# Kernel tuning notes

Hardware: AMD Instinct MI355X
Metric: run time of the kernel (lower is better)

Reference implementation:

```python
import jax, jax.numpy as jnp
import numpy as np

B, H, W, C = 16, 64, 64, 256
HEADS, WS, SHIFTS, QD = 8, 8, (0, 4), 512
N = WS * WS
HD = C // HEADS
MLP_H = 4 * C
DEPTH = 2
EPS = 1e-5


def _rel_pos_index():
    coords = np.stack(np.meshgrid(np.arange(WS), np.arange(WS), indexing='ij'))  # [2,ws,ws]
    flat = coords.reshape(2, -1)
    rel = (flat[:, :, None] - flat[:, None, :]).transpose(1, 2, 0)  # [N,N,2]
    rel[..., 0] += WS - 1
    rel[..., 1] += WS - 1
    rel[..., 0] *= 2 * WS - 1
    return jnp.asarray(rel.sum(-1))  # [N,N] int


def _shift_mask(shift):
    img = np.zeros((H, W))
    cnt = 0
    for hs in (slice(0, -WS), slice(-WS, -shift), slice(-shift, None)):
        for ws_ in (slice(0, -WS), slice(-WS, -shift), slice(-shift, None)):
            img[hs, ws_] = cnt
            cnt += 1
    mw = img.reshape(H // WS, WS, W // WS, WS).transpose(0, 2, 1, 3).reshape(-1, N)  # [nW,N]
    am = mw[:, None, :] - mw[:, :, None]
    return jnp.asarray(np.where(am != 0, -100.0, 0.0).astype(np.float32))  # [nW,N,N]


RPI = _rel_pos_index()


def layernorm(x, g, b):
    mu = x.mean(-1, keepdims=True)
    var = ((x - mu) ** 2).mean(-1, keepdims=True)
    return (x - mu) * jax.lax.rsqrt(var + EPS) * g + b


def window_partition(x):  # [B,H,W,C] -> [B*nW, N, C]
    x = x.reshape(B, H // WS, WS, W // WS, WS, C)
    return x.transpose(0, 1, 3, 2, 4, 5).reshape(-1, N, C)


def window_reverse(w):  # [B*nW, N, C] -> [B,H,W,C]
    x = w.reshape(B, H // WS, W // WS, WS, WS, C)
    return x.transpose(0, 1, 3, 2, 4, 5).reshape(B, H, W, C)


def swin_block(x, shift, n1g, n1b, qkvw, qkvb, rpb, pw, pb, n2g, n2b, f1w, f1b, f2w, f2b):
    shortcut = x
    y = layernorm(x, n1g, n1b).reshape(B, H, W, C)
    if shift > 0:
        y = jnp.roll(y, (-shift, -shift), axis=(1, 2))
    xw = window_partition(y)                                      # [B_, N, C]
    qkv = (xw @ qkvw + qkvb).reshape(-1, N, 3, HEADS, HD)
    q, k, v = (qkv[:, :, i].transpose(0, 2, 1, 3) for i in range(3))  # [B_,h,N,hd]
    scores = jnp.einsum('bhnd,bhmd->bhnm', q * (HD ** -0.5), k)
    bias = rpb[RPI].transpose(2, 0, 1)                            # [h,N,N]
    scores = scores + bias[None]
    if shift > 0:
        mask = _shift_mask(shift)                                 # [nW,N,N]
        nW = mask.shape[0]
        scores = scores.reshape(B, nW, HEADS, N, N) + mask[None, :, None]
        scores = scores.reshape(-1, HEADS, N, N)
    attn = jax.nn.softmax(scores, axis=-1)
    out = jnp.einsum('bhnm,bhmd->bhnd', attn, v).transpose(0, 2, 1, 3).reshape(-1, N, C)
    out = out @ pw + pb
    y = window_reverse(out)
    if shift > 0:
        y = jnp.roll(y, (shift, shift), axis=(1, 2))
    x = shortcut + y.reshape(B, H * W, C)
    h = layernorm(x, n2g, n2b)
    h = jax.nn.gelu(h @ f1w + f1b, approximate=False) @ f2w + f2b
    return x + h


def cross_attn(x, cond, cng, cnb, inw, inb, outw, outb):
    xn = layernorm(x, cng, cnb)
    q = xn @ inw[:C].T + inb[:C]
    k = cond @ inw[C:2 * C].T + inb[C:2 * C]
    v = cond @ inw[2 * C:].T + inb[2 * C:]
    Tq, Tk = q.shape[1], k.shape[1]
    q = q.reshape(B, Tq, HEADS, HD).transpose(0, 2, 1, 3) * (HD ** -0.5)
    k = k.reshape(B, Tk, HEADS, HD).transpose(0, 2, 1, 3)
    v = v.reshape(B, Tk, HEADS, HD).transpose(0, 2, 1, 3)
    a = jax.nn.softmax(jnp.einsum('bhqd,bhkd->bhqk', q, k), axis=-1)
    o = jnp.einsum('bhqk,bhkd->bhqd', a, v).transpose(0, 2, 1, 3).reshape(B, Tq, C)
    return x + o @ outw.T + outb


def setup_inputs() -> dict:
    key = jax.random.key(0)
    ks = iter(jax.random.split(key, 40))
    s = 0.02
    d = {
        'x': jax.random.normal(next(ks), (B, H * W, C), jnp.float32),
        'emb': jax.random.normal(next(ks), (B, 1, QD), jnp.float32),
        'qenc_w': jax.random.normal(next(ks), (QD, C)) * s,
        'qenc_b': jnp.zeros((C,)),
        'n1_g': jnp.ones((DEPTH, C)), 'n1_b': jnp.zeros((DEPTH, C)),
        'qkv_w': jax.random.normal(next(ks), (DEPTH, C, 3 * C)) * s,
        'qkv_b': jnp.zeros((DEPTH, 3 * C)),
        'rpb': jax.random.normal(next(ks), (DEPTH, (2 * WS - 1) ** 2, HEADS)) * s,
        'proj_w': jax.random.normal(next(ks), (DEPTH, C, C)) * s,
        'proj_b': jnp.zeros((DEPTH, C)),
        'n2_g': jnp.ones((DEPTH, C)), 'n2_b': jnp.zeros((DEPTH, C)),
        'fc1_w': jax.random.normal(next(ks), (DEPTH, C, MLP_H)) * s,
        'fc1_b': jnp.zeros((DEPTH, MLP_H)),
        'fc2_w': jax.random.normal(next(ks), (DEPTH, MLP_H, C)) * s,
        'fc2_b': jnp.zeros((DEPTH, C)),
        'cn_g': jnp.ones((DEPTH, C)), 'cn_b': jnp.zeros((DEPTH, C)),
        'ca_in_w': jax.random.normal(next(ks), (DEPTH, 3 * C, C)) * s,
        'ca_in_b': jnp.zeros((DEPTH, 3 * C)),
        'ca_out_w': jax.random.normal(next(ks), (DEPTH, C, C)) * s,
        'ca_out_b': jnp.zeros((DEPTH, C)),
    }
    return d


def reference(x, emb, qenc_w, qenc_b, n1_g, n1_b, qkv_w, qkv_b, rpb, proj_w, proj_b,
              n2_g, n2_b, fc1_w, fc1_b, fc2_w, fc2_b, cn_g, cn_b,
              ca_in_w, ca_in_b, ca_out_w, ca_out_b):
    for d in range(DEPTH):
        x = swin_block(x, SHIFTS[d], n1_g[d], n1_b[d], qkv_w[d], qkv_b[d], rpb[d],
                       proj_w[d], proj_b[d], n2_g[d], n2_b[d],
                       fc1_w[d], fc1_b[d], fc2_w[d], fc2_b[d])
        cond = emb @ qenc_w + qenc_b  # recomputed per block as in original
        x = cross_attn(x, cond, cn_g[d], cn_b[d], ca_in_w[d], ca_in_b[d],
                       ca_out_w[d], ca_out_b[d])
    return x
```

## Files before the change

kernel.cpp:

```cpp
#include <hip/hip_runtime.h>


typedef unsigned short bfraw;
typedef short s16x8 __attribute__((ext_vector_type(8)));
typedef short s16x4 __attribute__((ext_vector_type(4)));
typedef float f32x4 __attribute__((ext_vector_type(4)));

#define DEV static __device__ __forceinline__

DEV float b2f(int u){
  union { unsigned int i; float f; } x;
  x.i = ((unsigned int)u & 0xffffu) << 16;
  return x.f;
}
DEV unsigned short f2bbits(float f){
  union { float f; unsigned int i; } x; x.f = f;
  unsigned int i = x.i;
  unsigned int lsb = (i >> 16) & 1u;
  i += 0x7fffu + lsb;
  return (unsigned short)(i >> 16);
}
DEV float gelu_tanh(float x){
  float t2 = 1.5957691216057308f * fmaf(0.044715f * x * x, x, x);
  float e = __expf(-t2);
  return x * __builtin_amdgcn_rcpf(1.f + e);
}

#define GLOAD_LDS16(g, l) __builtin_amdgcn_global_load_lds(                      \
    (const __attribute__((address_space(1))) void*)(g),                          \
    (__attribute__((address_space(3))) void*)(l), 16, 0, 0)

__global__ void k_tr(const float* __restrict__ in, bfraw* __restrict__ out, int K, int N){
  int idx = blockIdx.x * 256 + threadIdx.x;
  if (idx >= K * N) return;
  int n = idx / K, k = idx - n * K;
  out[idx] = f2bbits(in[(size_t)k * N + n]);
}

__global__ __launch_bounds__(256) void k_ln(
    const float* __restrict__ x, const float* __restrict__ g,
    const float* __restrict__ b, bfraw* __restrict__ y)
{
  const int lane = threadIdx.x & 63, wv = threadIdx.x >> 6;
  const size_t row = (size_t)blockIdx.x * 4 + wv;
  const float4 v = *(const float4*)(x + row * 256 + lane * 4);
  float s  = v.x + v.y + v.z + v.w;
  float s2 = v.x*v.x + v.y*v.y + v.z*v.z + v.w*v.w;
#pragma unroll
  for (int off = 32; off; off >>= 1){
    s  += __shfl_xor(s,  off);
    s2 += __shfl_xor(s2, off);
  }
  float mu  = s * (1.f/256.f);
  float var = s2 * (1.f/256.f) - mu * mu;
  float rs  = rsqrtf(var + 1e-5f);
  const float4 gv = *(const float4*)(g + lane * 4);
  const float4 bv = *(const float4*)(b + lane * 4);
  s16x4 o;
  o[0] = (short)f2bbits((v.x - mu) * rs * gv.x + bv.x);
  o[1] = (short)f2bbits((v.y - mu) * rs * gv.y + bv.y);
  o[2] = (short)f2bbits((v.z - mu) * rs * gv.z + bv.z);
  o[3] = (short)f2bbits((v.w - mu) * rs * gv.w + bv.w);
  *(s16x4*)(y + row * 256 + lane * 4) = o;
}

template<int EPI>
__global__ __launch_bounds__(256, 2) void k_gemm(
    const bfraw* __restrict__ A, const bfraw* __restrict__ Bt,
    const float* __restrict__ bias,
    bfraw* __restrict__ Cout, int ldc,
    float* __restrict__ xfp, const float* __restrict__ xin,
    const float* __restrict__ addv,
    int M, int N, int K, int shift)
{
  constexpr int BK = 64;
  __shared__ __align__(16) bfraw sA[2][128 * BK];
  __shared__ __align__(16) bfraw sB[2][128 * BK];
  const int tid = threadIdx.x, lane = tid & 63, w = tid >> 6;
  const int lo16 = lane & 15, hg = lane >> 4;
  const int nbm = M >> 7, nbn = N >> 7;
  const int nwg = nbm * nbn;
  const int bid = blockIdx.x;
  const int wgid = (bid & 7) * (nwg >> 3) + (bid >> 3);
  const int tn = wgid % nbn, tm = wgid / nbn;
  const int m0 = tm << 7, n0 = tn << 7;
  const int wm = w & 1, wn = w >> 1;
  f32x4 acc[4][4] = {};

  const int srow = (w << 5) + (lane >> 3);
  const int scol = (((lane & 7) ^ (lane >> 3)) << 3);
  const int ksw  = (lane & 7) << 3;
  const bfraw* gA = A  + (size_t)(m0 + srow) * K + scol;
  const bfraw* gB = Bt + (size_t)(n0 + srow) * K + scol;

  const int cb = n0 + (wn << 6) + 4 * hg;

  f32x4 bv4[4];
#pragma unroll
  for (int ni = 0; ni < 4; ++ni) bv4[ni] = *(const f32x4*)(bias + cb + ni * 16);
  size_t rowoff_[4];
  f32x4 pre[16], pav[4];
  if constexpr (EPI == 2 || EPI == 3){
#pragma unroll
    for (int mi = 0; mi < 4; ++mi){
      const int r = m0 + (wm << 6) + (mi << 4) + lo16;
      if constexpr (EPI == 2){
        int b_ = r >> 12, rem = r & 4095;
        int wi = rem >> 6, n_ = rem & 63;
        int gi = ((wi >> 3) * 8 + (n_ >> 3) + shift) & 63;
        int gj = ((wi & 7) * 8 + (n_ & 7) + shift) & 63;
        rowoff_[mi] = ((size_t)b_ << 12) + gi * 64 + gj;
      } else {
        rowoff_[mi] = (size_t)r;
      }
      const float* src = (EPI == 2 ? xin : (const float*)xfp) + rowoff_[mi] * 256 + cb;
#pragma unroll
      for (int ni = 0; ni < 4; ++ni)
        pre[mi * 4 + ni] = *(const f32x4*)(src + ni * 16);
    }
    if constexpr (EPI == 3){
      const float* av = addv + (size_t)(m0 >> 12) * 256 + cb;
#pragma unroll
      for (int ni = 0; ni < 4; ++ni) pav[ni] = *(const f32x4*)(av + ni * 16);
    }
  }

  const int nt = K / BK;
#pragma unroll
  for (int i = 0; i < 4; ++i){
    GLOAD_LDS16(gA + (size_t)(i * 8) * K, &sA[0][(w * 4 + i) * 512]);
    GLOAD_LDS16(gB + (size_t)(i * 8) * K, &sB[0][(w * 4 + i) * 512]);
  }
  for (int t = 0; t < nt; ++t){
    __syncthreads();
    const int cur = t & 1;
    if (t + 1 < nt){
      const int nxt = cur ^ 1, kt = (t + 1) * BK;
#pragma unroll
      for (int i = 0; i < 4; ++i){
        GLOAD_LDS16(gA + (size_t)(i * 8) * K + kt, &sA[nxt][(w * 4 + i) * 512]);
        GLOAD_LDS16(gB + (size_t)(i * 8) * K + kt, &sB[nxt][(w * 4 + i) * 512]);
      }
    }
#pragma unroll
    for (int ks = 0; ks < 2; ++ks){
      const int ko = (ks * 32 + (hg << 3)) ^ ksw;
      s16x8 af[4], bfr[4];
#pragma unroll
      for (int i = 0; i < 4; ++i){
        af[i]  = *(const s16x8*)&sA[cur][((wm << 6) + (i << 4) + lo16) * BK + ko];
        bfr[i] = *(const s16x8*)&sB[cur][((wn << 6) + (i << 4) + lo16) * BK + ko];
      }
#pragma unroll
      for (int ni = 0; ni < 4; ++ni)
#pragma unroll
        for (int mi = 0; mi < 4; ++mi)
          acc[ni][mi] = __builtin_amdgcn_mfma_f32_16x16x32_bf16(
              bfr[ni], af[mi], acc[ni][mi], 0, 0, 0);
    }
  }

#pragma unroll
  for (int mi = 0; mi < 4; ++mi){
    if constexpr (EPI == 0 || EPI == 1){
      const int r = m0 + (wm << 6) + (mi << 4) + lo16;
      bfraw* crow = Cout + (size_t)r * ldc + cb;
#pragma unroll
      for (int ni = 0; ni < 4; ++ni){
        f32x4 v = acc[ni][mi] + bv4[ni];
        s16x4 o;
#pragma unroll
        for (int j = 0; j < 4; ++j){
          float val = v[j];
          if constexpr (EPI == 1) val = gelu_tanh(val);
          o[j] = (short)f2bbits(val);
        }
        *(s16x4*)(crow + ni * 16) = o;
      }
    } else if constexpr (EPI == 2){
      float* xo = xfp + rowoff_[mi] * 256 + cb;
#pragma unroll
      for (int ni = 0; ni < 4; ++ni)
        *(f32x4*)(xo + ni * 16) = acc[ni][mi] + bv4[ni] + pre[mi * 4 + ni];
    } else {
      float* xo = xfp + rowoff_[mi] * 256 + cb;
#pragma unroll
      for (int ni = 0; ni < 4; ++ni)
        *(f32x4*)(xo + ni * 16) = acc[ni][mi] + bv4[ni] + pre[mi * 4 + ni] + pav[ni];
    }
  }
}

__global__ __launch_bounds__(64) void k_bias(const float* __restrict__ rpb,
                                             float* __restrict__ biasPk)
{
  const int blk = blockIdx.x;
  const int d = blk >> 5, cls = (blk >> 3) & 3, h = blk & 7;
  const int l = threadIdx.x, lo16 = l & 15, hg = l >> 4;
  const float* rp = rpb + (size_t)d * 225 * 8;
  float* ob = biasPk + (((size_t)d * 4 + cls) * 8 + h) * 4096;
#pragma unroll
  for (int mi = 0; mi < 4; ++mi)
#pragma unroll
    for (int ni = 0; ni < 4; ++ni)
#pragma unroll
      for (int j = 0; j < 4; ++j){
        int k = 16 * mi + 4 * hg + j, q = 16 * ni + lo16;
        int qr = q >> 3, qc = q & 7, kr = k >> 3, kc = k & 7;
        float v = rp[((qr - kr + 7) * 15 + (qc - kc + 7)) * 8 + h];
        if (d == 1){
          int lq = ((cls >> 1) ? (qr < 4 ? 1 : 2) : 0) * 3 + ((cls & 1) ? (qc < 4 ? 1 : 2) : 0);
          int lk = ((cls >> 1) ? (kr < 4 ? 1 : 2) : 0) * 3 + ((cls & 1) ? (kc < 4 ? 1 : 2) : 0);
          if (lq != lk) v -= 100.f;
        }
        ob[(mi * 4 + ni) * 256 + l * 4 + j] = v;
      }
}

__global__ __launch_bounds__(64) void k_attn(
    const bfraw* __restrict__ qkv, const float* __restrict__ biasPk,
    bfraw* __restrict__ aout, int shift)
{
  __shared__ __align__(16) bfraw sV[64 * 32];
  __shared__ __align__(16) bfraw sP[64 * 64];
  const int win = blockIdx.x >> 3, h = blockIdx.x & 7;
  const int b = win >> 6, wr = (win >> 3) & 7, wc = win & 7;
  const int l = threadIdx.x, lo16 = l & 15, hg = l >> 4;

  auto grow_of = [&](int n) -> size_t {
    int gi = (wr * 8 + (n >> 3) + shift) & 63;
    int gj = (wc * 8 + (n & 7) + shift) & 63;
    return ((size_t)b << 12) + gi * 64 + gj;
  };

  s16x8 vreg[4];
#pragma unroll
  for (int i = 0; i < 4; ++i){
    int row = i * 16 + (l >> 2);
    vreg[i] = *(const s16x8*)(qkv + grow_of(row) * 768 + 512 + h * 32 + (l & 3) * 8);
  }
#pragma unroll
  for (int i = 0; i < 4; ++i)
    *(s16x8*)&sV[i * 512 + l * 8] = vreg[i];

  s16x8 aK[4], bQ[4];
#pragma unroll
  for (int t = 0; t < 4; ++t){
    const bfraw* base = qkv + grow_of(16 * t + lo16) * 768 + h * 32 + hg * 8;
    bQ[t] = *(const s16x8*)base;
    aK[t] = *(const s16x8*)(base + 256);
  }

  f32x4 acc[4][4] = {};
#pragma unroll
  for (int mi = 0; mi < 4; ++mi)
#pragma unroll
    for (int ni = 0; ni < 4; ++ni)
      acc[mi][ni] = __builtin_amdgcn_mfma_f32_16x16x32_bf16(aK[mi], bQ[ni], acc[mi][ni], 0, 0, 0);

  const int cls = ((wr == 7) ? 2 : 0) | ((wc == 7) ? 1 : 0);
  const float* bb = biasPk + ((size_t)(cls * 8 + h)) * 4096;
#pragma unroll
  for (int mi = 0; mi < 4; ++mi)
#pragma unroll
    for (int ni = 0; ni < 4; ++ni){
      f32x4 bv4 = *(const f32x4*)(bb + (mi * 4 + ni) * 256 + l * 4);
      acc[mi][ni] = acc[mi][ni] * 0.17677669529663689f + bv4;
    }

#pragma unroll
  for (int ni = 0; ni < 4; ++ni){
    float m = acc[0][ni][0];
#pragma unroll
    for (int mi = 0; mi < 4; ++mi)
#pragma unroll
      for (int j = 0; j < 4; ++j) m = fmaxf(m, acc[mi][ni][j]);
    m = fmaxf(m, __shfl_xor(m, 16));
    m = fmaxf(m, __shfl_xor(m, 32));
    float s = 0.f;
#pragma unroll
    for (int mi = 0; mi < 4; ++mi)
#pragma unroll
      for (int j = 0; j < 4; ++j){
        float e = __expf(acc[mi][ni][j] - m);
        acc[mi][ni][j] = e; s += e;
      }
    s += __shfl_xor(s, 16);
    s += __shfl_xor(s, 32);
    float inv = 1.f / s;
#pragma unroll
    for (int mi = 0; mi < 4; ++mi)
#pragma unroll
      for (int j = 0; j < 4; ++j) acc[mi][ni][j] *= inv;
  }

#pragma unroll
  for (int mi = 0; mi < 4; ++mi)
#pragma unroll
    for (int ni = 0; ni < 4; ++ni){
      unsigned int w0, w1;
      asm("v_cvt_pk_bf16_f32 %0, %1, %2" : "=v"(w0) : "v"(acc[mi][ni][0]), "v"(acc[mi][ni][1]));
      asm("v_cvt_pk_bf16_f32 %0, %1, %2" : "=v"(w1) : "v"(acc[mi][ni][2]), "v"(acc[mi][ni][3]));
      int q = 16 * ni + lo16;
      int ad = (q * 128 + (16 * mi + 4 * hg) * 2) ^ ((q & 7) << 4);
      *(uint2*)((char*)sP + ad) = make_uint2(w0, w1);
    }

  asm volatile("s_waitcnt lgkmcnt(0)" ::: "memory");
  __builtin_amdgcn_sched_barrier(0);

  f32x4 opv[4][2] = {};
#pragma unroll
  for (int kt = 0; kt < 2; ++kt){
    s16x8 ap[4];
#pragma unroll
    for (int qi = 0; qi < 4; ++qi){
      int q = 16 * qi + lo16;
      int ad = (q * 128 + (kt * 32 + hg * 8) * 2) ^ ((q & 7) << 4);
      ap[qi] = *(const s16x8*)((const char*)sP + ad);
    }
    s16x8 vb[2];
#pragma unroll
    for (int nt = 0; nt < 2; ++nt)
#pragma unroll
      for (int e = 0; e < 8; ++e)
        vb[nt][e] = (short)sV[(kt * 32 + hg * 8 + e) * 32 + nt * 16 + lo16];
#pragma unroll
    for (int qi = 0; qi < 4; ++qi)
#pragma unroll
      for (int nt = 0; nt < 2; ++nt)
        opv[qi][nt] = __builtin_amdgcn_mfma_f32_16x16x32_bf16(ap[qi], vb[nt], opv[qi][nt], 0, 0, 0);
  }

  bfraw* ob = aout + ((size_t)win * 64) * 256 + h * 32 + lo16;
#pragma unroll
  for (int qi = 0; qi < 4; ++qi)
#pragma unroll
    for (int nt = 0; nt < 2; ++nt)
#pragma unroll
      for (int j = 0; j < 4; ++j)
        ob[(size_t)(16 * qi + 4 * hg + j) * 256 + nt * 16] = f2bbits(opv[qi][nt][j]);
}

__global__ __launch_bounds__(256) void k_addvec(
    const float* __restrict__ emb, const float* __restrict__ qw, const float* __restrict__ qb,
    const float* __restrict__ inw, const float* __restrict__ inb,
    const float* __restrict__ outw, const float* __restrict__ outb,
    float* __restrict__ addv)
{
  const int d = blockIdx.x >> 4, b = blockIdx.x & 15;
  const int j = threadIdx.x;
  __shared__ float sc[256], sv[256];
  float a = qb[j];
  for (int k = 0; k < 512; ++k) a = fmaf(emb[b * 512 + k], qw[k * 256 + j], a);
  sc[j] = a; __syncthreads();
  float v = inb[d * 768 + 512 + j];
  const float* wrp = inw + (size_t)d * 768 * 256 + (size_t)(512 + j) * 256;
  for (int k = 0; k < 256; ++k) v = fmaf(sc[k], wrp[k], v);
  sv[j] = v; __syncthreads();
  float o = outb[d * 256 + j];
  const float* wop = outw + (size_t)d * 65536 + (size_t)j * 256;
  for (int k = 0; k < 256; ++k) o = fmaf(sv[k], wop[k], o);
  addv[(size_t)(d * 16 + b) * 256 + j] = o;
}

extern "C" void kernel_launch(void* const* d_in, const int* in_sizes, int n_in,
                              void* d_out, int out_size, void* d_ws, size_t ws_size,
                              hipStream_t stream)
{
  (void)in_sizes; (void)n_in; (void)out_size; (void)ws_size;
  const float* x_in     = (const float*)d_in[0];
  const float* emb      = (const float*)d_in[1];
  const float* qenc_w   = (const float*)d_in[2];
  const float* qenc_b   = (const float*)d_in[3];
  const float* n1_g     = (const float*)d_in[4];
  const float* n1_b     = (const float*)d_in[5];
  const float* qkv_w    = (const float*)d_in[6];
  const float* qkv_b    = (const float*)d_in[7];
  const float* rpb      = (const float*)d_in[8];
  const float* proj_w   = (const float*)d_in[9];
  const float* proj_b   = (const float*)d_in[10];
  const float* n2_g     = (const float*)d_in[11];
  const float* n2_b     = (const float*)d_in[12];
  const float* fc1_w    = (const float*)d_in[13];
  const float* fc1_b    = (const float*)d_in[14];
  const float* fc2_w    = (const float*)d_in[15];
  const float* fc2_b    = (const float*)d_in[16];
  const float* ca_in_w  = (const float*)d_in[19];
  const float* ca_in_b  = (const float*)d_in[20];
  const float* ca_out_w = (const float*)d_in[21];
  const float* ca_out_b = (const float*)d_in[22];

  float* xfp  = (float*)d_out;
  char* ws = (char*)d_ws;
  bfraw* ybuf = (bfraw*)ws;
  bfraw* qkvb = (bfraw*)(ws + ((size_t)32 << 20));
  bfraw* wT   = (bfraw*)(ws + ((size_t)160 << 20));
  float* biasPk = (float*)(ws + ((size_t)166 << 20));

  bfraw *qkvT[2], *projT[2], *fc1T[2], *fc2T[2];
  size_t off = 0;
  for (int d = 0; d < 2; ++d){ qkvT[d] = wT + off; off += 768 * 256; }
  for (int d = 0; d < 2; ++d){ projT[d] = wT + off; off += 256 * 256; }
  for (int d = 0; d < 2; ++d){ fc1T[d] = wT + off; off += 1024 * 256; }
  for (int d = 0; d < 2; ++d){ fc2T[d] = wT + off; off += 256 * 1024; }
  float* addv = (float*)(wT + ((off + 1) & ~(size_t)1));

  for (int d = 0; d < 2; ++d){
    k_tr<<<(256 * 768  + 255) / 256, 256, 0, stream>>>(qkv_w  + (size_t)d * 256 * 768,  qkvT[d], 256, 768);
    k_tr<<<(256 * 256  + 255) / 256, 256, 0, stream>>>(proj_w + (size_t)d * 256 * 256,  projT[d], 256, 256);
    k_tr<<<(256 * 1024 + 255) / 256, 256, 0, stream>>>(fc1_w  + (size_t)d * 256 * 1024, fc1T[d], 256, 1024);
    k_tr<<<(1024 * 256 + 255) / 256, 256, 0, stream>>>(fc2_w  + (size_t)d * 1024 * 256, fc2T[d], 1024, 256);
  }
  k_bias<<<64, 64, 0, stream>>>(rpb, biasPk);
  k_addvec<<<32, 256, 0, stream>>>(emb, qenc_w, qenc_b, ca_in_w, ca_in_b, ca_out_w, ca_out_b, addv);

  for (int d = 0; d < 2; ++d){
    const int shift = d ? 4 : 0;
    const float* resid_in = d ? (const float*)xfp : x_in;
    k_ln<<<16384, 256, 0, stream>>>(resid_in, n1_g + d * 256, n1_b + d * 256, ybuf);
    k_gemm<0><<<512 * 6, 256, 0, stream>>>(ybuf, qkvT[d], qkv_b + d * 768, qkvb, 768,
                                           nullptr, nullptr, nullptr, 65536, 768, 256, 0);
    k_attn<<<8192, 64, 0, stream>>>(qkvb, biasPk + (size_t)d * 4 * 8 * 4096, ybuf, shift);
    k_gemm<2><<<512 * 2, 256, 0, stream>>>(ybuf, projT[d], proj_b + d * 256, nullptr, 0,
                                           xfp, resid_in, nullptr, 65536, 256, 256, shift);
    k_ln<<<16384, 256, 0, stream>>>(xfp, n2_g + d * 256, n2_b + d * 256, ybuf);
    k_gemm<1><<<512 * 8, 256, 0, stream>>>(ybuf, fc1T[d], fc1_b + d * 1024, qkvb, 1024,
                                           nullptr, nullptr, nullptr, 65536, 1024, 256, 0);
    k_gemm<3><<<512 * 2, 256, 0, stream>>>(qkvb, fc2T[d], fc2_b + d * 256, nullptr, 0,
                                           xfp, nullptr, addv + (size_t)d * 16 * 256,
                                           65536, 256, 1024, 0);
  }
}
```

Measured before the change: 689.3 us.

## Single-buffer GEMM LDS tiles for higher occupancy and use packed bf16 conversion

The GEMM drops its double-buffered LDS tiles for a single buffer: each k-step now issues its global-to-LDS loads and waits on a second barrier before the MFMAs. LDS per block is halved and launch bounds are raised to request 4 blocks per CU, so latency is hidden by more resident waves rather than by software prefetch. Float-to-bf16 conversions in LayerNorm and the GEMM epilogue switch to the hardware packed convert instruction. The risk is that load latency is no longer overlapped within a block, and the tighter register budget could cause spills.

Result: slower. 865.4 us (+25.5%).

```diff
diff --git a/kernel.cpp b/kernel.cpp
--- a/kernel.cpp
+++ b/kernel.cpp
@@ -20,6 +20,11 @@
   i += 0x7fffu + lsb;
   return (unsigned short)(i >> 16);
 }
+DEV unsigned int pkbf(float lo, float hi){
+  unsigned int r;
+  asm("v_cvt_pk_bf16_f32 %0, %1, %2" : "=v"(r) : "v"(lo), "v"(hi));
+  return r;
+}
 DEV float gelu_tanh(float x){
   float t2 = 1.5957691216057308f * fmaf(0.044715f * x * x, x, x);
   float e = __expf(-t2);
@@ -56,16 +61,14 @@
   float rs  = rsqrtf(var + 1e-5f);
   const float4 gv = *(const float4*)(g + lane * 4);
   const float4 bv = *(const float4*)(b + lane * 4);
-  s16x4 o;
-  o[0] = (short)f2bbits((v.x - mu) * rs * gv.x + bv.x);
-  o[1] = (short)f2bbits((v.y - mu) * rs * gv.y + bv.y);
-  o[2] = (short)f2bbits((v.z - mu) * rs * gv.z + bv.z);
-  o[3] = (short)f2bbits((v.w - mu) * rs * gv.w + bv.w);
-  *(s16x4*)(y + row * 256 + lane * 4) = o;
+  uint2 o;
+  o.x = pkbf((v.x - mu) * rs * gv.x + bv.x, (v.y - mu) * rs * gv.y + bv.y);
+  o.y = pkbf((v.z - mu) * rs * gv.z + bv.z, (v.w - mu) * rs * gv.w + bv.w);
+  *(uint2*)(y + row * 256 + lane * 4) = o;
 }
 
 template<int EPI>
-__global__ __launch_bounds__(256, 2) void k_gemm(
+__global__ __launch_bounds__(256, 4) void k_gemm(
     const bfraw* __restrict__ A, const bfraw* __restrict__ Bt,
     const float* __restrict__ bias,
     bfraw* __restrict__ Cout, int ldc,
@@ -74,8 +77,8 @@
     int M, int N, int K, int shift)
 {
   constexpr int BK = 64;
-  __shared__ __align__(16) bfraw sA[2][128 * BK];
-  __shared__ __align__(16) bfraw sB[2][128 * BK];
+  __shared__ __align__(16) bfraw sA[128 * BK];
+  __shared__ __align__(16) bfraw sB[128 * BK];
   const int tid = threadIdx.x, lane = tid & 63, w = tid >> 6;
   const int lo16 = lane & 15, hg = lane >> 4;
   const int nbm = M >> 7, nbn = N >> 7;
@@ -125,31 +128,22 @@
     }
   }
 
-  const int nt = K / BK;
-#pragma unroll
-  for (int i = 0; i < 4; ++i){
-    GLOAD_LDS16(gA + (size_t)(i * 8) * K, &sA[0][(w * 4 + i) * 512]);
-    GLOAD_LDS16(gB + (size_t)(i * 8) * K, &sB[0][(w * 4 + i) * 512]);
-  }
-  for (int t = 0; t < nt; ++t){
+  for (int kt = 0; kt < K; kt += BK){
     __syncthreads();
-    const int cur = t & 1;
-    if (t + 1 < nt){
-      const int nxt = cur ^ 1, kt = (t + 1) * BK;
-#pragma unroll
-      for (int i = 0; i < 4; ++i){
-        GLOAD_LDS16(gA + (size_t)(i * 8) * K + kt, &sA[nxt][(w * 4 + i) * 512]);
-        GLOAD_LDS16(gB + (size_t)(i * 8) * K + kt, &sB[nxt][(w * 4 + i) * 512]);
-      }
-    }
+#pragma unroll
+    for (int i = 0; i < 4; ++i){
+      GLOAD_LDS16(gA + (size_t)(i * 8) * K + kt, &sA[(w * 4 + i) * 512]);
+      GLOAD_LDS16(gB + (size_t)(i * 8) * K + kt, &sB[(w * 4 + i) * 512]);
+    }
+    __syncthreads();
 #pragma unroll
     for (int ks = 0; ks < 2; ++ks){
       const int ko = (ks * 32 + (hg << 3)) ^ ksw;
       s16x8 af[4], bfr[4];
 #pragma unroll
       for (int i = 0; i < 4; ++i){
-        af[i]  = *(const s16x8*)&sA[cur][((wm << 6) + (i << 4) + lo16) * BK + ko];
-        bfr[i] = *(const s16x8*)&sB[cur][((wn << 6) + (i << 4) + lo16) * BK + ko];
+        af[i]  = *(const s16x8*)&sA[((wm << 6) + (i << 4) + lo16) * BK + ko];
+        bfr[i] = *(const s16x8*)&sB[((wn << 6) + (i << 4) + lo16) * BK + ko];
       }
 #pragma unroll
       for (int ni = 0; ni < 4; ++ni)
@@ -168,14 +162,12 @@
 #pragma unroll
       for (int ni = 0; ni < 4; ++ni){
         f32x4 v = acc[ni][mi] + bv4[ni];
-        s16x4 o;
-#pragma unroll
-        for (int j = 0; j < 4; ++j){
-          float val = v[j];
-          if constexpr (EPI == 1) val = gelu_tanh(val);
-          o[j] = (short)f2bbits(val);
+        if constexpr (EPI == 1){
+          v[0] = gelu_tanh(v[0]); v[1] = gelu_tanh(v[1]);
+          v[2] = gelu_tanh(v[2]); v[3] = gelu_tanh(v[3]);
         }
-        *(s16x4*)(crow + ni * 16) = o;
+        uint2 o = make_uint2(pkbf(v[0], v[1]), pkbf(v[2], v[3]));
+        *(uint2*)(crow + ni * 16) = o;
       }
     } else if constexpr (EPI == 2){
       float* xo = xfp + rowoff_[mi] * 256 + cb;
@@ -298,9 +290,8 @@
   for (int mi = 0; mi < 4; ++mi)
 #pragma unroll
     for (int ni = 0; ni < 4; ++ni){
-      unsigned int w0, w1;
-      asm("v_cvt_pk_bf16_f32 %0, %1, %2" : "=v"(w0) : "v"(acc[mi][ni][0]), "v"(acc[mi][ni][1]));
-      asm("v_cvt_pk_bf16_f32 %0, %1, %2" : "=v"(w1) : "v"(acc[mi][ni][2]), "v"(acc[mi][ni][3]));
+      unsigned int w0 = pkbf(acc[mi][ni][0], acc[mi][ni][1]);
+      unsigned int w1 = pkbf(acc[mi][ni][2], acc[mi][ni][3]);
       int q = 16 * ni + lo16;
       int ad = (q * 128 + (16 * mi + 4 * hg) * 2) ^ ((q & 7) << 4);
       *(uint2*)((char*)sP + ad) = make_uint2(w0, w1);
```
